# Kernel optimization log

Hardware: AMD Instinct MI355X
Metric: run time of the kernel (lower is better)

The kernel has to match this reference:

```python
import jax, jax.numpy as jnp
import numpy as np

ALPHA = 0.5
BETA = 0.5
SMOOTH = 1e-08


def setup_inputs() -> dict:
    key = jax.random.key(0)
    k1, k2 = jax.random.split(key)
    B, C, H, W = 8, 19, 512, 512
    pred = jax.random.normal(k1, (B, C, H, W), dtype=jnp.float32)
    target = jax.random.randint(k2, (B, H, W), 0, C, dtype=jnp.int32)
    return {"pred": pred, "target": target}


def reference(pred, target):
    B, C, H, W = pred.shape
    p = jax.nn.softmax(pred, axis=1)                       # [B,C,H,W]
    # one-hot target along class axis: [B,C,H,W]
    t = (target[:, None, :, :] == jnp.arange(C, dtype=target.dtype)[None, :, None, None]).astype(p.dtype)
    tp = jnp.einsum('bchw,bchw->bc', p, t)                 # true positives
    sum_p = jnp.sum(p, axis=(2, 3))                        # [B,C]
    sum_t = jnp.sum(t, axis=(2, 3))                        # [B,C]
    fp = sum_p - tp
    fn = sum_t - tp
    tversky = (tp + SMOOTH) / (tp + ALPHA * fp + BETA * fn + SMOOTH)
    return jnp.mean(1.0 - tversky)
```

## Files before the change

kernel.cpp:

```cpp
#include <hip/hip_runtime.h>

#define NC 19
#define NB 8
#define HW (512 * 512)
#define SMOOTH 1e-8f
#define THREADS 256
#define NBINS 8
#define NBC (NB * NC)


__global__ __launch_bounds__(THREADS, 8) void tversky_pass1(
        const float* __restrict__ pred, const int* __restrict__ tgt,
        float* __restrict__ acc) {
    const int b   = blockIdx.y;
    const int tid = threadIdx.x;

    __shared__ float lds_tp[NC];
    __shared__ float lds_red[THREADS / 64][NC];

    if (tid < NC) lds_tp[tid] = 0.0f;
    __syncthreads();

    const int px = blockIdx.x * THREADS + tid;
    const float* pp = pred + (size_t)b * NC * HW + px;
    const int    t  = tgt[(size_t)b * HW + px];

    float e[NC];
    float s = 0.0f;
#pragma unroll
    for (int c = 0; c < NC; ++c) {
        e[c] = __expf(pp[(size_t)c * HW]);
        s += e[c];
    }
    const float iv = 1.0f / s;

    float tp = 0.0f;
#pragma unroll
    for (int c = 0; c < NC; ++c) {
        const float p = e[c] * iv;
        tp   = (t == c) ? p : tp;
        e[c] = p + ((t == c) ? 1.0f : 0.0f);
    }

    atomicAdd(&lds_tp[t], tp);

#pragma unroll
    for (int c = 0; c < NC; ++c) {
#pragma unroll
        for (int off = 1; off < 64; off <<= 1)
            e[c] += __shfl_xor(e[c], off, 64);
    }

    const int wave = tid >> 6;
    if ((tid & 63) == 0) {
#pragma unroll
        for (int c = 0; c < NC; ++c) lds_red[wave][c] = e[c];
    }
    __syncthreads();

    if (tid < NC) {
        float spc = 0.0f;
#pragma unroll
        for (int w = 0; w < THREADS / 64; ++w) spc += lds_red[w][tid];
        float* base = acc + (blockIdx.x & (NBINS - 1)) * (2 * NBC);
        atomicAdd(&base[b * NC + tid], lds_tp[tid]);
        atomicAdd(&base[NBC + b * NC + tid], spc);
    }
}

__global__ __launch_bounds__(256) void tversky_pass2(const float* __restrict__ acc,
                                                     float* __restrict__ out) {
    __shared__ float red[256];
    const int i = threadIdx.x;
    float v = 0.0f;
    if (i < NBC) {
        float tp = 0.0f, spc = 0.0f;
#pragma unroll
        for (int bin = 0; bin < NBINS; ++bin) {
            tp  += acc[bin * 2 * NBC + i];
            spc += acc[bin * 2 * NBC + NBC + i];
        }
        const float tv = (tp + SMOOTH) / (0.5f * spc + SMOOTH);
        v = 1.0f - tv;
    }
    red[i] = v;
    __syncthreads();
    for (int s = 128; s > 0; s >>= 1) {
        if (i < s) red[i] += red[i + s];
        __syncthreads();
    }
    if (i == 0) out[0] = red[0] / (float)NBC;
}

extern "C" void kernel_launch(void* const* d_in, const int* in_sizes, int n_in,
                              void* d_out, int out_size, void* d_ws, size_t ws_size,
                              hipStream_t stream) {
    const float* pred = (const float*)d_in[0];
    const int*   tgt  = (const int*)d_in[1];
    float* acc = (float*)d_ws;
    float* out = (float*)d_out;

    hipMemsetAsync(acc, 0, NBINS * 2 * NBC * sizeof(float), stream);

    dim3 grid(HW / THREADS, NB);
    tversky_pass1<<<grid, THREADS, 0, stream>>>(pred, tgt, acc);

    tversky_pass2<<<1, 256, 0, stream>>>(acc, out);
}
```

Baseline: 230.2 us.

## Process multiple pixels per thread and accumulate before wave reduction

Each thread now loops over 8 pixels, accumulating per-class sums in registers, so the expensive 19-class shuffle reduction, LDS writes and global atomics run once per 8 pixels instead of once per pixel. The grid shrinks accordingly. Prediction loads become nontemporal to avoid polluting cache with streaming data. With the loop not unrolled, fewer loads are in flight per thread, which may reduce memory-level parallelism, and the smaller grid gives fewer blocks.

```diff
diff --git a/kernel.cpp b/kernel.cpp
--- a/kernel.cpp
+++ b/kernel.cpp
@@ -5,6 +5,7 @@
 #define HW (512 * 512)
 #define SMOOTH 1e-8f
 #define THREADS 256
+#define PXT 8
 #define NBINS 8
 #define NBC (NB * NC)
 
@@ -21,40 +22,50 @@
     if (tid < NC) lds_tp[tid] = 0.0f;
     __syncthreads();
 
-    const int px = blockIdx.x * THREADS + tid;
-    const float* pp = pred + (size_t)b * NC * HW + px;
-    const int    t  = tgt[(size_t)b * HW + px];
+    const float* pb = pred + (size_t)b * NC * HW;
+    const int*   tb = tgt  + (size_t)b * HW;
+    const int block_base = blockIdx.x * (THREADS * PXT);
 
-    float e[NC];
-    float s = 0.0f;
+    float a1[NC];
 #pragma unroll
-    for (int c = 0; c < NC; ++c) {
-        e[c] = __expf(pp[(size_t)c * HW]);
-        s += e[c];
+    for (int c = 0; c < NC; ++c) a1[c] = 0.0f;
+
+#pragma unroll 1
+    for (int p = 0; p < PXT; ++p) {
+        const int px = block_base + p * THREADS + tid;
+        const float* pp = pb + px;
+        const int t = tb[px];
+
+        float e[NC];
+        float s = 0.0f;
+#pragma unroll
+        for (int c = 0; c < NC; ++c) {
+            e[c] = __expf(__builtin_nontemporal_load(pp + (size_t)c * HW));
+            s += e[c];
+        }
+        const float iv = 1.0f / s;
+
+        float pt = 0.0f;
+#pragma unroll
+        for (int c = 0; c < NC; ++c) {
+            const float pc = e[c] * iv;
+            pt = (t == c) ? pc : pt;
+            a1[c] += pc + ((t == c) ? 1.0f : 0.0f);
+        }
+        atomicAdd(&lds_tp[t], pt);
     }
-    const float iv = 1.0f / s;
-
-    float tp = 0.0f;
-#pragma unroll
-    for (int c = 0; c < NC; ++c) {
-        const float p = e[c] * iv;
-        tp   = (t == c) ? p : tp;
-        e[c] = p + ((t == c) ? 1.0f : 0.0f);
-    }
-
-    atomicAdd(&lds_tp[t], tp);
 
 #pragma unroll
     for (int c = 0; c < NC; ++c) {
 #pragma unroll
         for (int off = 1; off < 64; off <<= 1)
-            e[c] += __shfl_xor(e[c], off, 64);
+            a1[c] += __shfl_xor(a1[c], off, 64);
     }
 
     const int wave = tid >> 6;
     if ((tid & 63) == 0) {
 #pragma unroll
-        for (int c = 0; c < NC; ++c) lds_red[wave][c] = e[c];
+        for (int c = 0; c < NC; ++c) lds_red[wave][c] = a1[c];
     }
     __syncthreads();
 
@@ -102,7 +113,7 @@
 
     hipMemsetAsync(acc, 0, NBINS * 2 * NBC * sizeof(float), stream);
 
-    dim3 grid(HW / THREADS, NB);
+    dim3 grid(HW / (THREADS * PXT), NB);
     tversky_pass1<<<grid, THREADS, 0, stream>>>(pred, tgt, acc);
 
     tversky_pass2<<<1, 256, 0, stream>>>(acc, out);
```

Result: faster. 223.0 us (-3.1%).
